# Kernel optimization log

Measured on AMD Instinct MI355X. Metric: run time of the kernel, lower is better.

Reference implementation:

```python
import jax, jax.numpy as jnp
import numpy as np

EMB_DIM = 2048
N_HEADS = 16
N_KV = 4
HEAD_DIM = 128
SEQ = 4096
BATCH = 1
ROPE_BASE = 10000.0
EPS = 1e-6
NEG = -1e9


def setup_inputs() -> dict:
    key = jax.random.key(0)
    ks = jax.random.split(key, 6)
    x = jax.random.normal(ks[0], (BATCH, SEQ, EMB_DIM), dtype=jnp.float32)
    position_ids = jnp.broadcast_to(jnp.arange(SEQ, dtype=jnp.int64 if jax.config.jax_enable_x64 else jnp.int32), (BATCH, SEQ))
    # additive causal mask
    causal = jnp.triu(jnp.full((SEQ, SEQ), NEG, dtype=jnp.float32), k=1)
    attn_mask = causal[None, None, :, :]
    sc = 0.02
    Wq = jax.random.normal(ks[1], (EMB_DIM, N_HEADS * HEAD_DIM), dtype=jnp.float32) * sc
    Wk = jax.random.normal(ks[2], (EMB_DIM, N_KV * HEAD_DIM), dtype=jnp.float32) * sc
    Wv = jax.random.normal(ks[3], (EMB_DIM, N_KV * HEAD_DIM), dtype=jnp.float32) * sc
    Wo = jax.random.normal(ks[4], (N_HEADS * HEAD_DIM, EMB_DIM), dtype=jnp.float32) * sc
    q_norm_w = jnp.ones((HEAD_DIM,), dtype=jnp.float32)
    k_norm_w = jnp.ones((HEAD_DIM,), dtype=jnp.float32)
    return {"x": x, "position_ids": position_ids, "attn_mask": attn_mask,
            "Wq": Wq, "Wk": Wk, "Wv": Wv, "Wo": Wo,
            "q_norm_w": q_norm_w, "k_norm_w": k_norm_w}


def _rmsnorm(x, w):
    dt = x.dtype
    xf = x.astype(jnp.float32)
    xf = xf * jax.lax.rsqrt(jnp.mean(xf * xf, axis=-1, keepdims=True) + EPS)
    return w * xf.astype(dt)


def _rope(x, position_ids):
    # x: [b, h, s, d]; position_ids: [b, s]
    half = HEAD_DIM // 2
    freqs = 1.0 / (ROPE_BASE ** (jnp.arange(0, HEAD_DIM, 2, dtype=jnp.float32) / HEAD_DIM))
    ang = position_ids.astype(jnp.float32)[..., None] * freqs  # [b, s, d/2]
    ang = jnp.concatenate([ang, ang], axis=-1)                  # [b, s, d]
    cos = jnp.cos(ang)[:, None, :, :].astype(x.dtype)
    sin = jnp.sin(ang)[:, None, :, :].astype(x.dtype)
    x1, x2 = x[..., :half], x[..., half:]
    rotated = jnp.concatenate([-x2, x1], axis=-1)
    return x * cos + rotated * sin


def reference(x, position_ids, attn_mask, Wq, Wk, Wv, Wo, q_norm_w, k_norm_w):
    b, s, _ = x.shape
    group = N_HEADS // N_KV
    Q = (x @ Wq).reshape(b, s, N_HEADS, HEAD_DIM).transpose(0, 2, 1, 3)  # [b,nh,s,d]
    K = (x @ Wk).reshape(b, s, N_KV, HEAD_DIM).transpose(0, 2, 1, 3)     # [b,nk,s,d]
    V = (x @ Wv).reshape(b, s, N_KV, HEAD_DIM).transpose(0, 2, 1, 3)
    Q = _rmsnorm(Q, q_norm_w)
    K = _rmsnorm(K, k_norm_w)
    Q = _rope(Q, position_ids)
    K = _rope(K, position_ids)
    new_kv_cache = (K, V)
    # GQA: group query heads instead of physically repeating K/V
    Qg = Q.reshape(b, N_KV, group, s, HEAD_DIM)
    scores = jnp.einsum('bkgqd,bkld->bkgql', Qg, K) / (HEAD_DIM ** 0.5)
    scores = scores + attn_mask[:, :, None, :, :]
    attn = jax.nn.softmax(scores.astype(jnp.float32), axis=-1).astype(x.dtype)
    ctx = jnp.einsum('bkgql,bkld->bkgqd', attn, V)          # [b,nk,g,s,d]
    ctx = ctx.reshape(b, N_HEADS, s, HEAD_DIM).transpose(0, 2, 1, 3).reshape(b, s, N_HEADS * HEAD_DIM)
    output = ctx @ Wo
    return (output, new_kv_cache[0], new_kv_cache[1])
```

## Files before the change

kernel.cpp:

```cpp
#include <hip/hip_runtime.h>
#include <hip/hip_bf16.h>

#define SEQ   4096
#define EMB   2048
#define NH    16
#define NKV   4
#define HD    128

typedef short  bf16x8 __attribute__((ext_vector_type(8)));
typedef float  f32x4  __attribute__((ext_vector_type(4)));

__device__ __forceinline__ unsigned short f2b(float f) {
    unsigned int u = __float_as_uint(f);
    unsigned int r = u + 0x7fffu + ((u >> 16) & 1u);
    return (unsigned short)(r >> 16);
}

__global__ void k_cvt_bf16(const float* __restrict__ in, unsigned short* __restrict__ out, int n) {
    int i = (blockIdx.x * blockDim.x + threadIdx.x) * 4;
    if (i >= n) return;
    float4 v = *(const float4*)(in + i);
    ushort4 o;
    o.x = f2b(v.x); o.y = f2b(v.y); o.z = f2b(v.z); o.w = f2b(v.w);
    *(ushort4*)(out + i) = o;
}

__global__ __launch_bounds__(256) void k_transpose_bf16(const float* __restrict__ W,
                                                        unsigned short* __restrict__ Wt,
                                                        int K, int N) {
    __shared__ float t[32][33];
    const int bk = blockIdx.x * 32, bn = blockIdx.y * 32;
    const int col = threadIdx.x & 31, rq = threadIdx.x >> 5;
#pragma unroll
    for (int i = 0; i < 4; ++i) {
        int r = rq + i * 8;
        t[r][col] = W[(size_t)(bk + r) * N + bn + col];
    }
    __syncthreads();
#pragma unroll
    for (int i = 0; i < 4; ++i) {
        int r = rq + i * 8;
        Wt[(size_t)(bn + r) * K + bk + col] = f2b(t[col][r]);
    }
}

__global__ __launch_bounds__(256) void k_gemm_bf16(
    const unsigned short* __restrict__ A, const unsigned short* __restrict__ Bt,
    float* __restrict__ C, int M, int N, int K) {
    __shared__ unsigned short As[128][72];
    __shared__ unsigned short Bs[128][72];
    const int tid  = threadIdx.x;
    const int w    = tid >> 6, lane = tid & 63;
    const int wr   = w >> 1,   wc   = w & 1;
    const int lr   = lane & 15, lg  = lane >> 4;
    const int bx   = blockIdx.x, by = blockIdx.y;

    f32x4 acc[4][4] = {};
    const int nkt = K >> 6;
    for (int kt = 0; kt < nkt; ++kt) {
#pragma unroll
        for (int i = 0; i < 4; ++i) {
            int c   = tid + i * 256;
            int row = c >> 3, col = (c & 7) * 8;
            *(int4*)&As[row][col] = *(const int4*)(A  + (size_t)(by * 128 + row) * K + kt * 64 + col);
            *(int4*)&Bs[row][col] = *(const int4*)(Bt + (size_t)(bx * 128 + row) * K + kt * 64 + col);
        }
        __syncthreads();
#pragma unroll
        for (int kk = 0; kk < 2; ++kk) {
            bf16x8 a[4], b[4];
#pragma unroll
            for (int mi = 0; mi < 4; ++mi)
                a[mi] = *(const bf16x8*)&As[wr * 64 + mi * 16 + lr][kk * 32 + lg * 8];
#pragma unroll
            for (int ni = 0; ni < 4; ++ni)
                b[ni] = *(const bf16x8*)&Bs[wc * 64 + ni * 16 + lr][kk * 32 + lg * 8];
#pragma unroll
            for (int mi = 0; mi < 4; ++mi)
#pragma unroll
                for (int ni = 0; ni < 4; ++ni)
                    acc[mi][ni] = __builtin_amdgcn_mfma_f32_16x16x32_bf16(a[mi], b[ni], acc[mi][ni], 0, 0, 0);
        }
        __syncthreads();
    }
#pragma unroll
    for (int mi = 0; mi < 4; ++mi)
#pragma unroll
        for (int ni = 0; ni < 4; ++ni)
#pragma unroll
            for (int r = 0; r < 4; ++r) {
                int row = by * 128 + wr * 64 + mi * 16 + lg * 4 + r;
                int col = bx * 128 + wc * 64 + ni * 16 + lr;
                C[(size_t)row * N + col] = acc[mi][ni][r];
            }
}

__global__ void k_qnorm_rope(const float* __restrict__ Qp, const int* __restrict__ pos,
                             const float* __restrict__ qw, unsigned short* __restrict__ Qb) {
    int row  = blockIdx.x * 4 + (threadIdx.x >> 6);
    int lane = threadIdx.x & 63;
    int s = row >> 4, h = row & 15;
    const float* src = Qp + (size_t)s * 2048 + h * 128;
    float x1 = src[lane], x2 = src[lane + 64];
    float ss = x1 * x1 + x2 * x2;
#pragma unroll
    for (int d = 1; d < 64; d <<= 1) ss += __shfl_xor(ss, d);
    float rs = rsqrtf(ss * (1.0f / 128.0f) + 1e-6f);
    float n1 = x1 * rs * qw[lane], n2 = x2 * rs * qw[lane + 64];
    float p = (float)pos[s];
    float freq = expf(-(float)lane * (9.210340371976184f / 64.0f));
    float ang = p * freq;
    float sn, c;
    sincosf(ang, &sn, &c);
    const float SC = 0.08838834764831845f;
    float o1 = (n1 * c - n2 * sn) * SC;
    float o2 = (n2 * c + n1 * sn) * SC;
    unsigned short* dst = Qb + ((size_t)h * SEQ + s) * HD;
    dst[lane]      = f2b(o1);
    dst[lane + 64] = f2b(o2);
}

__global__ void k_knorm_rope(const float* __restrict__ Kp, const int* __restrict__ pos,
                             const float* __restrict__ kw, unsigned short* __restrict__ Kb,
                             float* __restrict__ outK) {
    int row  = blockIdx.x * 4 + (threadIdx.x >> 6);
    int lane = threadIdx.x & 63;
    int s = row >> 2, kv = row & 3;
    const float* src = Kp + (size_t)s * 512 + kv * 128;
    float x1 = src[lane], x2 = src[lane + 64];
    float ss = x1 * x1 + x2 * x2;
#pragma unroll
    for (int d = 1; d < 64; d <<= 1) ss += __shfl_xor(ss, d);
    float rs = rsqrtf(ss * (1.0f / 128.0f) + 1e-6f);
    float n1 = x1 * rs * kw[lane], n2 = x2 * rs * kw[lane + 64];
    float p = (float)pos[s];
    float freq = expf(-(float)lane * (9.210340371976184f / 64.0f));
    float ang = p * freq;
    float sn, c;
    sincosf(ang, &sn, &c);
    float o1 = n1 * c - n2 * sn;
    float o2 = n2 * c + n1 * sn;
    unsigned short* dst = Kb + ((size_t)kv * SEQ + s) * HD;
    float* od = outK + ((size_t)kv * SEQ + s) * HD;
    dst[lane]      = f2b(o1);
    dst[lane + 64] = f2b(o2);
    od[lane]       = o1;
    od[lane + 64]  = o2;
}

__global__ void k_vpack(const float* __restrict__ Vp, unsigned short* __restrict__ Vtb,
                        float* __restrict__ outV) {
    int tid = blockIdx.x * 256 + threadIdx.x;
    int s = tid >> 9, c = tid & 511;
    int kv = c >> 7, d = c & 127;
    float v = Vp[tid];
    Vtb[((size_t)kv * HD + d) * SEQ + s] = f2b(v);
    outV[((size_t)kv * SEQ + s) * HD + d] = v;
}

__global__ __launch_bounds__(256) void k_flash(
    const unsigned short* __restrict__ Qb, const unsigned short* __restrict__ Kb,
    const unsigned short* __restrict__ Vtb, unsigned short* __restrict__ ctxb) {
    __shared__ unsigned short Pl[4][16][80];
    const int bid = blockIdx.x;
    const int h  = bid & 15, kv = h >> 2;
    const int qt = 63 - (bid >> 4);
    const int qb = qt * 64;
    const int w  = threadIdx.x >> 6, lane = threadIdx.x & 63;
    const int lr = lane & 15, lg = lane >> 4;

    const unsigned short* Qh = Qb + ((size_t)h * SEQ + qb + w * 16) * HD;
    bf16x8 aq[4];
#pragma unroll
    for (int kk = 0; kk < 4; ++kk)
        aq[kk] = *(const bf16x8*)(Qh + (size_t)lr * HD + kk * 32 + lg * 8);

    f32x4 O[8] = {};
    float m = -1e30f, l = 0.0f;

    const int nt = qt + 1;
    const unsigned short* Kh = Kb  + (size_t)kv * SEQ * HD;
    const unsigned short* Vh = Vtb + (size_t)kv * HD * SEQ;

    for (int t = 0; t < nt; ++t) {
        const int kvB = t * 64;
        f32x4 S[4];
#pragma unroll
        for (int ni = 0; ni < 4; ++ni) {
            f32x4 s = {};
#pragma unroll
            for (int kk = 0; kk < 4; ++kk) {
                bf16x8 bk = *(const bf16x8*)(Kh + (size_t)(kvB + ni * 16 + lr) * HD + kk * 32 + lg * 8);
                s = __builtin_amdgcn_mfma_f32_16x16x32_bf16(bk, aq[kk], s, 0, 0, 0);
            }
            S[ni] = s;
        }
        if (t == nt - 1) {
            const int q = qb + w * 16 + lr;
#pragma unroll
            for (int ni = 0; ni < 4; ++ni)
#pragma unroll
                for (int r = 0; r < 4; ++r) {
                    int key = kvB + ni * 16 + lg * 4 + r;
                    if (key > q) S[ni][r] = -1e30f;
                }
        }
        float pmax = -1e30f;
#pragma unroll
        for (int ni = 0; ni < 4; ++ni)
#pragma unroll
            for (int r = 0; r < 4; ++r) pmax = fmaxf(pmax, S[ni][r]);
        pmax = fmaxf(pmax, __shfl_xor(pmax, 16));
        pmax = fmaxf(pmax, __shfl_xor(pmax, 32));
        float mn = fmaxf(m, pmax);
        float al = __expf(m - mn);
        m = mn;
        float su = 0.0f;
#pragma unroll
        for (int ni = 0; ni < 4; ++ni)
#pragma unroll
            for (int r = 0; r < 4; ++r) {
                float pp = __expf(S[ni][r] - mn);
                S[ni][r] = pp;
                su += pp;
            }
        su += __shfl_xor(su, 16);
        su += __shfl_xor(su, 32);
        l = l * al + su;

#pragma unroll
        for (int ni = 0; ni < 4; ++ni) {
            unsigned int w0 = (unsigned int)f2b(S[ni][0]) | ((unsigned int)f2b(S[ni][1]) << 16);
            unsigned int w1 = (unsigned int)f2b(S[ni][2]) | ((unsigned int)f2b(S[ni][3]) << 16);
            *(unsigned int*)&Pl[w][lr][ni * 16 + lg * 4]     = w0;
            *(unsigned int*)&Pl[w][lr][ni * 16 + lg * 4 + 2] = w1;
        }
        float alq[4];
#pragma unroll
        for (int r = 0; r < 4; ++r) alq[r] = __shfl(al, lg * 4 + r);
#pragma unroll
        for (int dt = 0; dt < 8; ++dt)
#pragma unroll
            for (int r = 0; r < 4; ++r) O[dt][r] *= alq[r];

#pragma unroll
        for (int kk = 0; kk < 2; ++kk) {
            bf16x8 pa = *(const bf16x8*)&Pl[w][lr][kk * 32 + lg * 8];
#pragma unroll
            for (int dt = 0; dt < 8; ++dt) {
                bf16x8 bv = *(const bf16x8*)(Vh + (size_t)(dt * 16 + lr) * SEQ + kvB + kk * 32 + lg * 8);
                O[dt] = __builtin_amdgcn_mfma_f32_16x16x32_bf16(pa, bv, O[dt], 0, 0, 0);
            }
        }
    }
#pragma unroll
    for (int r = 0; r < 4; ++r) {
        float li = __shfl(l, lg * 4 + r);
        float inv = 1.0f / li;
        int row = qb + w * 16 + lg * 4 + r;
#pragma unroll
        for (int dt = 0; dt < 8; ++dt) {
            int col = h * HD + dt * 16 + lr;
            ctxb[(size_t)row * (NH * HD) + col] = f2b(O[dt][r] * inv);
        }
    }
}

extern "C" void kernel_launch(void* const* d_in, const int* in_sizes, int n_in,
                              void* d_out, int out_size, void* d_ws, size_t ws_size,
                              hipStream_t stream) {
    const float* x   = (const float*)d_in[0];
    const int*   pos = (const int*)d_in[1];
    const float* Wq  = (const float*)d_in[3];
    const float* Wk  = (const float*)d_in[4];
    const float* Wv  = (const float*)d_in[5];
    const float* Wo  = (const float*)d_in[6];
    const float* qw  = (const float*)d_in[7];
    const float* kw  = (const float*)d_in[8];

    float* out  = (float*)d_out;
    float* outK = out + (size_t)SEQ * EMB;
    float* outV = outK + (size_t)NKV * SEQ * HD;

    char* ws = (char*)d_ws;
    float*          Qp   = (float*)(ws + 0);
    float*          Kp   = (float*)(ws + 33554432);
    float*          Vp   = (float*)(ws + 41943040);
    unsigned short* xb   = (unsigned short*)(ws + 50331648);
    unsigned short* Wqt  = (unsigned short*)(ws + 67108864);
    unsigned short* Wkt  = (unsigned short*)(ws + 75497472);
    unsigned short* Wvt  = (unsigned short*)(ws + 77594624);
    unsigned short* Wot  = (unsigned short*)(ws + 79691776);
    unsigned short* Qb   = (unsigned short*)(ws + 88080384);
    unsigned short* Kb   = (unsigned short*)(ws + 104857600);
    unsigned short* Vtb  = (unsigned short*)(ws + 109051904);
    unsigned short* ctxb = (unsigned short*)(ws + 113246208);

    k_cvt_bf16<<<8192, 256, 0, stream>>>(x, xb, SEQ * EMB);
    k_transpose_bf16<<<dim3(64, 64), 256, 0, stream>>>(Wq, Wqt, 2048, 2048);
    k_transpose_bf16<<<dim3(64, 16), 256, 0, stream>>>(Wk, Wkt, 2048, 512);
    k_transpose_bf16<<<dim3(64, 16), 256, 0, stream>>>(Wv, Wvt, 2048, 512);
    k_transpose_bf16<<<dim3(64, 64), 256, 0, stream>>>(Wo, Wot, 2048, 2048);

    k_gemm_bf16<<<dim3(16, 32), 256, 0, stream>>>(xb, Wqt, Qp, SEQ, 2048, 2048);
    k_gemm_bf16<<<dim3(4, 32),  256, 0, stream>>>(xb, Wkt, Kp, SEQ, 512, 2048);
    k_gemm_bf16<<<dim3(4, 32),  256, 0, stream>>>(xb, Wvt, Vp, SEQ, 512, 2048);

    k_qnorm_rope<<<(SEQ * NH) / 4, 256, 0, stream>>>(Qp, pos, qw, Qb);
    k_knorm_rope<<<(SEQ * NKV) / 4, 256, 0, stream>>>(Kp, pos, kw, Kb, outK);
    k_vpack<<<(SEQ * NKV * HD) / 256, 256, 0, stream>>>(Vp, Vtb, outV);

    k_flash<<<1024, 256, 0, stream>>>(Qb, Kb, Vtb, ctxb);

    k_gemm_bf16<<<dim3(16, 32), 256, 0, stream>>>(ctxb, Wot, out, SEQ, 2048, 2048);
}
```

Before: 846.6 us.

## Use direct global-to-LDS loads in GEMM and pipeline K/V loads in flash attention

The GEMM now stages its A and B tiles with global_load_lds instead of a register round-trip, and it drops the padded LDS layout, which may bring back bank conflicts on the MFMA operand reads. The flash kernel double-buffers K fragments in registers so the next tile's loads are issued during the current softmax. It also hoists V loads ahead of the P write. Each block now handles two query tiles, q-tile p and 63-p, to balance causal work, heads are mapped with an XCD-aware scheme, and the grid is halved with launch_bounds(256,2). The extra register use for the K and V buffers may limit occupancy.

```diff
diff --git a/kernel.cpp b/kernel.cpp
--- a/kernel.cpp
+++ b/kernel.cpp
@@ -15,6 +15,10 @@
     unsigned int r = u + 0x7fffu + ((u >> 16) & 1u);
     return (unsigned short)(r >> 16);
 }
+
+#define GLOAD_LDS16(gp, lp) \
+    __builtin_amdgcn_global_load_lds((const __attribute__((address_space(1))) unsigned int*)(gp), \
+                                     (__attribute__((address_space(3))) unsigned int*)(lp), 16, 0, 0)
 
 __global__ void k_cvt_bf16(const float* __restrict__ in, unsigned short* __restrict__ out, int n) {
     int i = (blockIdx.x * blockDim.x + threadIdx.x) * 4;
@@ -47,23 +51,25 @@
 __global__ __launch_bounds__(256) void k_gemm_bf16(
     const unsigned short* __restrict__ A, const unsigned short* __restrict__ Bt,
     float* __restrict__ C, int M, int N, int K) {
-    __shared__ unsigned short As[128][72];
-    __shared__ unsigned short Bs[128][72];
+    __shared__ unsigned short As[128 * 64];
+    __shared__ unsigned short Bs[128 * 64];
     const int tid  = threadIdx.x;
     const int w    = tid >> 6, lane = tid & 63;
     const int wr   = w >> 1,   wc   = w & 1;
     const int lr   = lane & 15, lg  = lane >> 4;
     const int bx   = blockIdx.x, by = blockIdx.y;
 
+    const int srow = w * 32 + (lane >> 3);
+    const int scol = (lane & 7) * 8;
+
     f32x4 acc[4][4] = {};
     const int nkt = K >> 6;
     for (int kt = 0; kt < nkt; ++kt) {
 #pragma unroll
         for (int i = 0; i < 4; ++i) {
-            int c   = tid + i * 256;
-            int row = c >> 3, col = (c & 7) * 8;
-            *(int4*)&As[row][col] = *(const int4*)(A  + (size_t)(by * 128 + row) * K + kt * 64 + col);
-            *(int4*)&Bs[row][col] = *(const int4*)(Bt + (size_t)(bx * 128 + row) * K + kt * 64 + col);
+            const int row = srow + i * 8;
+            GLOAD_LDS16(A  + (size_t)(by * 128 + row) * K + kt * 64 + scol, &As[(w * 4 + i) * 512]);
+            GLOAD_LDS16(Bt + (size_t)(bx * 128 + row) * K + kt * 64 + scol, &Bs[(w * 4 + i) * 512]);
         }
         __syncthreads();
 #pragma unroll
@@ -71,10 +77,10 @@
             bf16x8 a[4], b[4];
 #pragma unroll
             for (int mi = 0; mi < 4; ++mi)
-                a[mi] = *(const bf16x8*)&As[wr * 64 + mi * 16 + lr][kk * 32 + lg * 8];
+                a[mi] = *(const bf16x8*)&As[(wr * 64 + mi * 16 + lr) * 64 + kk * 32 + lg * 8];
 #pragma unroll
             for (int ni = 0; ni < 4; ++ni)
-                b[ni] = *(const bf16x8*)&Bs[wc * 64 + ni * 16 + lr][kk * 32 + lg * 8];
+                b[ni] = *(const bf16x8*)&Bs[(wc * 64 + ni * 16 + lr) * 64 + kk * 32 + lg * 8];
 #pragma unroll
             for (int mi = 0; mi < 4; ++mi)
 #pragma unroll
@@ -158,110 +164,118 @@
     outV[((size_t)kv * SEQ + s) * HD + d] = v;
 }
 
-__global__ __launch_bounds__(256) void k_flash(
+
+#define LOADK(tt, kd) do { const int _kvB = (tt) * 64; \
+    _Pragma("unroll") for (int ni = 0; ni < 4; ++ni) \
+    _Pragma("unroll") for (int kk = 0; kk < 4; ++kk) \
+        kd[ni][kk] = *(const bf16x8*)(Kh + (size_t)(_kvB + ni * 16 + lr) * HD + kk * 32 + lg * 8); \
+} while (0)
+
+#define FSTEP(kc, kn) do { \
+    const int kvB = t * 64; \
+    f32x4 S[4]; \
+    _Pragma("unroll") for (int ni = 0; ni < 4; ++ni) { \
+        f32x4 s = {}; \
+        _Pragma("unroll") for (int kk = 0; kk < 4; ++kk) \
+            s = __builtin_amdgcn_mfma_f32_16x16x32_bf16(kc[ni][kk], aq[kk], s, 0, 0, 0); \
+        S[ni] = s; \
+    } \
+    if (t + 1 < nt) LOADK(t + 1, kn); \
+    if (t == nt - 1) { \
+        const int q = qb + w * 16 + lr; \
+        _Pragma("unroll") for (int ni = 0; ni < 4; ++ni) \
+        _Pragma("unroll") for (int r = 0; r < 4; ++r) { \
+            int key = kvB + ni * 16 + lg * 4 + r; \
+            if (key > q) S[ni][r] = -1e30f; \
+        } \
+    } \
+    float pmax = -1e30f; \
+    _Pragma("unroll") for (int ni = 0; ni < 4; ++ni) \
+    _Pragma("unroll") for (int r = 0; r < 4; ++r) pmax = fmaxf(pmax, S[ni][r]); \
+    pmax = fmaxf(pmax, __shfl_xor(pmax, 16)); \
+    pmax = fmaxf(pmax, __shfl_xor(pmax, 32)); \
+    float mn = fmaxf(m, pmax); \
+    float al = __expf(m - mn); \
+    m = mn; \
+    float su = 0.0f; \
+    _Pragma("unroll") for (int ni = 0; ni < 4; ++ni) \
+    _Pragma("unroll") for (int r = 0; r < 4; ++r) { \
+        float pp = __expf(S[ni][r] - mn); S[ni][r] = pp; su += pp; \
+    } \
+    su += __shfl_xor(su, 16); \
+    su += __shfl_xor(su, 32); \
+    l = l * al + su; \
+    _Pragma("unroll") for (int dt = 0; dt < 8; ++dt) \
+    _Pragma("unroll") for (int k2 = 0; k2 < 2; ++k2) \
+        vr[dt][k2] = *(const bf16x8*)(Vh + (size_t)(dt * 16 + lr) * SEQ + kvB + k2 * 32 + lg * 8); \
+    _Pragma("unroll") for (int ni = 0; ni < 4; ++ni) { \
+        unsigned int w0 = (unsigned int)f2b(S[ni][0]) | ((unsigned int)f2b(S[ni][1]) << 16); \
+        unsigned int w1 = (unsigned int)f2b(S[ni][2]) | ((unsigned int)f2b(S[ni][3]) << 16); \
+        *(unsigned int*)&Pl[w][lr][ni * 16 + lg * 4]     = w0; \
+        *(unsigned int*)&Pl[w][lr][ni * 16 + lg * 4 + 2] = w1; \
+    } \
+    float alq[4]; \
+    _Pragma("unroll") for (int r = 0; r < 4; ++r) alq[r] = __shfl(al, lg * 4 + r); \
+    _Pragma("unroll") for (int dt = 0; dt < 8; ++dt) \
+    _Pragma("unroll") for (int r = 0; r < 4; ++r) O[dt][r] *= alq[r]; \
+    _Pragma("unroll") for (int k2 = 0; k2 < 2; ++k2) { \
+        bf16x8 pa = *(const bf16x8*)&Pl[w][lr][k2 * 32 + lg * 8]; \
+        _Pragma("unroll") for (int dt = 0; dt < 8; ++dt) \
+            O[dt] = __builtin_amdgcn_mfma_f32_16x16x32_bf16(pa, vr[dt][k2], O[dt], 0, 0, 0); \
+    } \
+} while (0)
+
+__global__ __launch_bounds__(256, 2) void k_flash(
     const unsigned short* __restrict__ Qb, const unsigned short* __restrict__ Kb,
     const unsigned short* __restrict__ Vtb, unsigned short* __restrict__ ctxb) {
     __shared__ unsigned short Pl[4][16][80];
     const int bid = blockIdx.x;
-    const int h  = bid & 15, kv = h >> 2;
-    const int qt = 63 - (bid >> 4);
-    const int qb = qt * 64;
+    const int xcd = bid & 7, g = bid >> 3;
+    const int h  = xcd * 2 + (g & 1);
+    const int p  = g >> 1;
+    const int kv = h >> 2;
     const int w  = threadIdx.x >> 6, lane = threadIdx.x & 63;
     const int lr = lane & 15, lg = lane >> 4;
 
-    const unsigned short* Qh = Qb + ((size_t)h * SEQ + qb + w * 16) * HD;
-    bf16x8 aq[4];
-#pragma unroll
-    for (int kk = 0; kk < 4; ++kk)
-        aq[kk] = *(const bf16x8*)(Qh + (size_t)lr * HD + kk * 32 + lg * 8);
-
-    f32x4 O[8] = {};
-    float m = -1e30f, l = 0.0f;
-
-    const int nt = qt + 1;
     const unsigned short* Kh = Kb  + (size_t)kv * SEQ * HD;
     const unsigned short* Vh = Vtb + (size_t)kv * HD * SEQ;
 
-    for (int t = 0; t < nt; ++t) {
-        const int kvB = t * 64;
-        f32x4 S[4];
-#pragma unroll
-        for (int ni = 0; ni < 4; ++ni) {
-            f32x4 s = {};
-#pragma unroll
-            for (int kk = 0; kk < 4; ++kk) {
-                bf16x8 bk = *(const bf16x8*)(Kh + (size_t)(kvB + ni * 16 + lr) * HD + kk * 32 + lg * 8);
-                s = __builtin_amdgcn_mfma_f32_16x16x32_bf16(bk, aq[kk], s, 0, 0, 0);
+    bf16x8 kA[4][4], kB[4][4], vr[8][2];
+
+#pragma unroll 1
+    for (int phase = 0; phase < 2; ++phase) {
+        const int qt = phase ? (63 - p) : p;
+        const int qb = qt * 64;
+        const int nt = qt + 1;
+
+        const unsigned short* Qh = Qb + ((size_t)h * SEQ + qb + w * 16) * HD;
+        bf16x8 aq[4];
+#pragma unroll
+        for (int kk = 0; kk < 4; ++kk)
+            aq[kk] = *(const bf16x8*)(Qh + (size_t)lr * HD + kk * 32 + lg * 8);
+
+        f32x4 O[8] = {};
+        float m = -1e30f, l = 0.0f;
+
+        LOADK(0, kA);
+        int t = 0;
+        while (true) {
+            FSTEP(kA, kB);
+            if (++t == nt) break;
+            FSTEP(kB, kA);
+            if (++t == nt) break;
+        }
+
+#pragma unroll
+        for (int r = 0; r < 4; ++r) {
+            float li = __shfl(l, lg * 4 + r);
+            float inv = 1.0f / li;
+            int row = qb + w * 16 + lg * 4 + r;
+#pragma unroll
+            for (int dt = 0; dt < 8; ++dt) {
+                int col = h * HD + dt * 16 + lr;
+                ctxb[(size_t)row * (NH * HD) + col] = f2b(O[dt][r] * inv);
             }
-            S[ni] = s;
-        }
-        if (t == nt - 1) {
-            const int q = qb + w * 16 + lr;
-#pragma unroll
-            for (int ni = 0; ni < 4; ++ni)
-#pragma unroll
-                for (int r = 0; r < 4; ++r) {
-                    int key = kvB + ni * 16 + lg * 4 + r;
-                    if (key > q) S[ni][r] = -1e30f;
-                }
-        }
-        float pmax = -1e30f;
-#pragma unroll
-        for (int ni = 0; ni < 4; ++ni)
-#pragma unroll
-            for (int r = 0; r < 4; ++r) pmax = fmaxf(pmax, S[ni][r]);
-        pmax = fmaxf(pmax, __shfl_xor(pmax, 16));
-        pmax = fmaxf(pmax, __shfl_xor(pmax, 32));
-        float mn = fmaxf(m, pmax);
-        float al = __expf(m - mn);
-        m = mn;
-        float su = 0.0f;
-#pragma unroll
-        for (int ni = 0; ni < 4; ++ni)
-#pragma unroll
-            for (int r = 0; r < 4; ++r) {
-                float pp = __expf(S[ni][r] - mn);
-                S[ni][r] = pp;
-                su += pp;
-            }
-        su += __shfl_xor(su, 16);
-        su += __shfl_xor(su, 32);
-        l = l * al + su;
-
-#pragma unroll
-        for (int ni = 0; ni < 4; ++ni) {
-            unsigned int w0 = (unsigned int)f2b(S[ni][0]) | ((unsigned int)f2b(S[ni][1]) << 16);
-            unsigned int w1 = (unsigned int)f2b(S[ni][2]) | ((unsigned int)f2b(S[ni][3]) << 16);
-            *(unsigned int*)&Pl[w][lr][ni * 16 + lg * 4]     = w0;
-            *(unsigned int*)&Pl[w][lr][ni * 16 + lg * 4 + 2] = w1;
-        }
-        float alq[4];
-#pragma unroll
-        for (int r = 0; r < 4; ++r) alq[r] = __shfl(al, lg * 4 + r);
-#pragma unroll
-        for (int dt = 0; dt < 8; ++dt)
-#pragma unroll
-            for (int r = 0; r < 4; ++r) O[dt][r] *= alq[r];
-
-#pragma unroll
-        for (int kk = 0; kk < 2; ++kk) {
-            bf16x8 pa = *(const bf16x8*)&Pl[w][lr][kk * 32 + lg * 8];
-#pragma unroll
-            for (int dt = 0; dt < 8; ++dt) {
-                bf16x8 bv = *(const bf16x8*)(Vh + (size_t)(dt * 16 + lr) * SEQ + kvB + kk * 32 + lg * 8);
-                O[dt] = __builtin_amdgcn_mfma_f32_16x16x32_bf16(pa, bv, O[dt], 0, 0, 0);
-            }
-        }
-    }
-#pragma unroll
-    for (int r = 0; r < 4; ++r) {
-        float li = __shfl(l, lg * 4 + r);
-        float inv = 1.0f / li;
-        int row = qb + w * 16 + lg * 4 + r;
-#pragma unroll
-        for (int dt = 0; dt < 8; ++dt) {
-            int col = h * HD + dt * 16 + lr;
-            ctxb[(size_t)row * (NH * HD) + col] = f2b(O[dt][r] * inv);
         }
     }
 }
@@ -310,7 +324,7 @@
     k_knorm_rope<<<(SEQ * NKV) / 4, 256, 0, stream>>>(Kp, pos, kw, Kb, outK);
     k_vpack<<<(SEQ * NKV * HD) / 256, 256, 0, stream>>>(Vp, Vtb, outV);
 
-    k_flash<<<1024, 256, 0, stream>>>(Qb, Kb, Vtb, ctxb);
+    k_flash<<<512, 256, 0, stream>>>(Qb, Kb, Vtb, ctxb);
 
     k_gemm_bf16<<<dim3(16, 32), 256, 0, stream>>>(ctxb, Wot, out, SEQ, 2048, 2048);
 }
```

Result: slower. 945.0 us (+11.6%).
